# Optimization experiments

Hardware: AMD Instinct MI355X
Metric: run time of the kernel (lower is better)

Reference implementation:

```python
import jax, jax.numpy as jnp
import numpy as np

BSZ, H, P, L = 8, 512, 128, 8192
DT_MIN, DT_MAX = 1e-3, 1e-1


def setup_inputs() -> dict:
    key = jax.random.key(0)
    ks = jax.random.split(key, 6)
    inp = {}
    inp["input_sequence"] = jax.random.normal(ks[0], (BSZ, 1, H, 1, L), jnp.float32)
    # HiPPO-like init: negative real parts, pi*k imaginary parts
    inp["Lambda_re"] = -jax.random.uniform(ks[1], (P,), jnp.float32, 0.1, 1.0)
    inp["Lambda_im"] = jnp.pi * jnp.arange(P, dtype=jnp.float32)
    # lecun_normal-ish: fan_in = H for B, fan_in = P for C (real+imag parts)
    inp["B"] = jax.random.normal(ks[2], (P, H, 2), jnp.float32) / np.float32(np.sqrt(2 * H))
    inp["C"] = jax.random.normal(ks[3], (H, P, 2), jnp.float32) / np.float32(np.sqrt(2 * P))
    inp["D"] = jax.random.normal(ks[4], (H,), jnp.float32)
    u01 = jax.random.uniform(ks[5], (P, 1), jnp.float32)
    inp["log_step"] = u01 * np.float32(np.log(DT_MAX) - np.log(DT_MIN)) + np.float32(np.log(DT_MIN))
    return inp


def _binary_operator(q_i, q_j):
    A_i, b_i = q_i
    A_j, b_j = q_j
    return (A_j * A_i, A_j * b_i + b_j)


def reference(input_sequence, Lambda_re, Lambda_im, B, C, D, log_step):
    # (bsz, 1, H, 1, L) -> (bsz, L, H)
    u = input_sequence[:, 0, :, 0].transpose(0, 2, 1)

    Lambda = Lambda_re + 1j * Lambda_im                      # (P,)
    B_tilde = B[..., 0] + 1j * B[..., 1]                     # (P, H)
    C_tilde = C[..., 0] + 1j * C[..., 1]                     # (H, P)
    step = jnp.exp(log_step[:, 0])                           # (P,)

    # zero-order hold discretization
    Lambda_bar = jnp.exp(Lambda * step)                      # (P,)
    B_bar = ((Lambda_bar - 1.0) / Lambda)[:, None] * B_tilde # (P, H)

    Bu = jnp.einsum('blh,ph->blp', u, B_bar)                 # (bsz, L, P) complex
    Lambda_elems = jnp.broadcast_to(Lambda_bar, Bu.shape)
    _, xs = jax.lax.associative_scan(_binary_operator, (Lambda_elems, Bu), axis=1)

    # conj_sym=True -> factor of 2 on the real part of emissions
    ys = 2.0 * jnp.einsum('blp,hp->blh', xs, C_tilde).real + D * u
    ys = jax.nn.gelu(ys, approximate=False)

    # back to (bsz, 1, H, 1, L)
    return ys.transpose(0, 2, 1)[:, None, :, None, :]
```

## Files before the change

### kernel.cpp

```cpp
#include <hip/hip_runtime.h>
#include <hip/hip_bf16.h>
#include <cmath>

namespace {
constexpr int Pn = 128;
constexpr int Hn = 512;
constexpr int Ln = 8192;
constexpr int BS = 8;
constexpr size_t OFF_BMAT = 2048;
constexpr size_t OFF_CMAT = 264192;
constexpr size_t OFF_END  = 526336;
constexpr size_t OFF_CAR  = 2623488;
constexpr size_t HEADB    = 4720640;
constexpr size_t SZ_BU = (size_t)256 * Ln * 4;
}

typedef __attribute__((ext_vector_type(4))) float f32x4;
typedef __attribute__((ext_vector_type(8))) short bf16x8;
typedef __attribute__((ext_vector_type(4))) short bf16x4;

static __device__ inline short f2bf(float x) {
  __hip_bfloat16 h = __float2bfloat16(x);
  return *(short*)&h;
}

static __device__ inline void async_copy16(const void* g, void* l) {
  __builtin_amdgcn_global_load_lds(
      (const __attribute__((address_space(1))) unsigned int*)g,
      (__attribute__((address_space(3))) unsigned int*)l, 16, 0, 0);
}

__global__ void precompute_kernel(const float* __restrict__ Lre,
                                  const float* __restrict__ Lim,
                                  const float* __restrict__ Bin,
                                  const float* __restrict__ Cin,
                                  const float* __restrict__ lstep,
                                  float* __restrict__ Lam,
                                  __hip_bfloat16* __restrict__ Bmat,
                                  __hip_bfloat16* __restrict__ Cmat) {
  int tid = blockIdx.x * blockDim.x + threadIdx.x;
  if (tid < 2 * Pn * Hn) {
    int r = tid >> 9;
    int h = tid & (Hn - 1);
    int p = r & (Pn - 1);
    float st = expf(lstep[p]);
    float lr = Lre[p], li = Lim[p];
    float er = expf(lr * st);
    float cr = er * cosf(li * st);
    float ci = er * sinf(li * st);
    float nr = cr - 1.0f, ni = ci;
    float inv = 1.0f / (lr * lr + li * li);
    float wr = (nr * lr + ni * li) * inv;
    float wi = (ni * lr - nr * li) * inv;
    float btr = Bin[(p * Hn + h) * 2 + 0];
    float bti = Bin[(p * Hn + h) * 2 + 1];
    float val = (r < Pn) ? (wr * btr - wi * bti) : (wr * bti + wi * btr);
    Bmat[tid] = __float2bfloat16(val);
  } else if (tid < 4 * Pn * Hn) {
    int j = tid - 2 * Pn * Hn;
    int h = j >> 8;
    int c = j & 255;
    int p = c & (Pn - 1);
    float v = (c < Pn) ? 2.0f * Cin[(h * Pn + p) * 2 + 0]
                       : -2.0f * Cin[(h * Pn + p) * 2 + 1];
    Cmat[j] = __float2bfloat16(v);
  } else if (tid < 4 * Pn * Hn + 512) {
    int j = tid - 4 * Pn * Hn;
    int p = j & 127;
    int sel = j >> 7;
    float st = expf(lstep[p]);
    float lr = Lre[p], li = Lim[p];
    float sc = (sel < 2) ? st : 32.0f * st;
    float er = expf(lr * sc);
    Lam[(sel >> 1) * 256 + (sel & 1) * 128 + p] =
        (sel & 1) ? er * sinf(li * sc) : er * cosf(li * sc);
  }
}

__global__ __launch_bounds__(256) void gemm1_kernel(
    const __hip_bfloat16* __restrict__ Amat,
    const float* __restrict__ U,
    float* __restrict__ Bu,
    int b0) {
  __shared__ __align__(16) short As[256 * 32];
  __shared__ __align__(16) short Bs[64 * 40];
  const int t = threadIdx.x;
  const int lane = t & 63, w = t >> 6;
  const int n0 = blockIdx.x * 64;
  const int bz = blockIdx.z;
  const float* Ub = U + (size_t)(b0 + bz) * Hn * Ln;

  const int srow = lane >> 2, scol = (lane & 3) * 16;
  const int bn = t & 63, bkg = t >> 6;

  f32x4 acc[4][4] = {};
  for (int k0 = 0; k0 < Hn; k0 += 32) {
#pragma unroll
    for (int I2 = 0; I2 < 4; I2++) {
      int I = 4 * w + I2;
      async_copy16((const char*)(Amat + (size_t)(16 * I + srow) * Hn + k0) + scol,
                   (char*)As + I * 1024);
    }
    {
      float v[8];
#pragma unroll
      for (int j = 0; j < 8; j++)
        v[j] = Ub[(size_t)(k0 + bkg * 8 + j) * Ln + n0 + bn];
      bf16x8 pk;
#pragma unroll
      for (int j = 0; j < 8; j++) pk[j] = f2bf(v[j]);
      *(bf16x8*)&Bs[bn * 40 + bkg * 8] = pk;
    }
    __syncthreads();
    bf16x8 af[4], bfr[4];
#pragma unroll
    for (int mt = 0; mt < 4; mt++)
      af[mt] = *(const bf16x8*)&As[(64 * w + 16 * mt + (lane & 15)) * 32 + (lane >> 4) * 8];
#pragma unroll
    for (int nt = 0; nt < 4; nt++)
      bfr[nt] = *(const bf16x8*)&Bs[(16 * nt + (lane & 15)) * 40 + (lane >> 4) * 8];
#pragma unroll
    for (int mt = 0; mt < 4; mt++)
#pragma unroll
      for (int nt = 0; nt < 4; nt++)
        acc[mt][nt] = __builtin_amdgcn_mfma_f32_16x16x32_bf16(
            af[mt], bfr[nt], acc[mt][nt], 0, 0, 0);
    __syncthreads();
  }
  const int row4 = (lane >> 4) * 4, col = lane & 15;
  float* Bub = Bu + (size_t)bz * Ln * 256;
#pragma unroll
  for (int mt = 0; mt < 4; mt++)
#pragma unroll
    for (int nt = 0; nt < 4; nt++) {
      int n = n0 + 16 * nt + col;
      int m = 64 * w + 16 * mt + row4;
      *(f32x4*)&Bub[(size_t)n * 256 + m] = acc[mt][nt];
    }
}

__global__ __launch_bounds__(256) void scan_ends_kernel(const float* __restrict__ Bu,
                                                        const float* __restrict__ Lam,
                                                        float* __restrict__ End) {
  const int bz = blockIdx.y;
  const int t = threadIdx.x;
  const int c = blockIdx.x * 2 + (t >> 7);
  const int p = t & 127;
  const float Ar = Lam[p], Ai = Lam[128 + p];
  const float* base = Bu + ((size_t)bz * Ln + (size_t)c * 32) * 256;
  float br[32], bi[32];
#pragma unroll
  for (int i = 0; i < 32; i++) br[i] = base[(size_t)i * 256 + p];
#pragma unroll
  for (int i = 0; i < 32; i++) bi[i] = base[(size_t)i * 256 + 128 + p];
  float xr = 0.f, xi = 0.f;
#pragma unroll
  for (int i = 0; i < 32; i++) {
    float nr = fmaf(Ar, xr, fmaf(-Ai, xi, br[i]));
    float ni = fmaf(Ar, xi, fmaf(Ai, xr, bi[i]));
    xr = nr; xi = ni;
  }
  float* E = End + ((size_t)bz * 256 + c) * 256;
  E[p] = xr;
  E[128 + p] = xi;
}

__global__ __launch_bounds__(128) void carry_kernel(const float* __restrict__ End,
                                                    float* __restrict__ Carry,
                                                    const float* __restrict__ Lam) {
  const int bz = blockIdx.x;
  const int p = threadIdx.x;
  const float a32r = Lam[256 + p], a32i = Lam[384 + p];
  const float* E = End + (size_t)bz * 256 * 256;
  float* C = Carry + (size_t)bz * 256 * 256;
  float xr = 0.f, xi = 0.f;
  float er0[4], ei0[4], er1[4], ei1[4];
#pragma unroll
  for (int q = 0; q < 4; q++) {
    er0[q] = E[(size_t)q * 256 + p];
    ei0[q] = E[(size_t)q * 256 + 128 + p];
  }
  for (int c0 = 0; c0 < 256; c0 += 8) {
#pragma unroll
    for (int q = 0; q < 4; q++) {
      er1[q] = E[(size_t)(c0 + 4 + q) * 256 + p];
      ei1[q] = E[(size_t)(c0 + 4 + q) * 256 + 128 + p];
    }
#pragma unroll
    for (int q = 0; q < 4; q++) {
      C[(size_t)(c0 + q) * 256 + p] = xr;
      C[(size_t)(c0 + q) * 256 + 128 + p] = xi;
      float nr = fmaf(a32r, xr, fmaf(-a32i, xi, er0[q]));
      float ni = fmaf(a32r, xi, fmaf(a32i, xr, ei0[q]));
      xr = nr; xi = ni;
    }
#pragma unroll
    for (int q = 0; q < 4; q++) {
      int cn = c0 + 8 + q;
      if (cn < 256) {
        er0[q] = E[(size_t)cn * 256 + p];
        ei0[q] = E[(size_t)cn * 256 + 128 + p];
      }
    }
#pragma unroll
    for (int q = 0; q < 4; q++) {
      C[(size_t)(c0 + 4 + q) * 256 + p] = xr;
      C[(size_t)(c0 + 4 + q) * 256 + 128 + p] = xi;
      float nr = fmaf(a32r, xr, fmaf(-a32i, xi, er1[q]));
      float ni = fmaf(a32r, xi, fmaf(a32i, xr, ei1[q]));
      xr = nr; xi = ni;
    }
  }
}

__global__ __launch_bounds__(256) void scan_apply_kernel(float* __restrict__ Bu,
                                                         const float* __restrict__ Lam,
                                                         const float* __restrict__ Carry) {
  const int bz = blockIdx.y;
  const int t = threadIdx.x;
  const int c = blockIdx.x * 2 + (t >> 7);
  const int p = t & 127;
  const float Ar = Lam[p], Ai = Lam[128 + p];
  float* base = Bu + ((size_t)bz * Ln + (size_t)c * 32) * 256;
  const float* Cg = Carry + ((size_t)bz * 256 + c) * 256;
  float br[32], bi[32];
#pragma unroll
  for (int i = 0; i < 32; i++) br[i] = base[(size_t)i * 256 + p];
#pragma unroll
  for (int i = 0; i < 32; i++) bi[i] = base[(size_t)i * 256 + 128 + p];
  float xr = Cg[p], xi = Cg[128 + p];
#pragma unroll
  for (int i = 0; i < 32; i++) {
    float nr = fmaf(Ar, xr, fmaf(-Ai, xi, br[i]));
    float ni = fmaf(Ar, xi, fmaf(Ai, xr, bi[i]));
    xr = nr; xi = ni;
    base[(size_t)i * 256 + p] = nr;
    base[(size_t)i * 256 + 128 + p] = ni;
  }
}

__global__ __launch_bounds__(256) void gemm2_kernel(
    const __hip_bfloat16* __restrict__ Cmat,
    const float* __restrict__ Xs,
    const float* __restrict__ U,
    const float* __restrict__ Dv,
    float* __restrict__ Out, int b0) {
  __shared__ __align__(16) short As[128 * 32];
  __shared__ __align__(16) short Bs[128 * 40];
  const int t = threadIdx.x;
  const int lane = t & 63, w = t >> 6;
  const int wm = w >> 1, wn = w & 1;
  const int n0 = blockIdx.x * 128;
  const int m0 = blockIdx.y * 128;
  const int bz = blockIdx.z;
  const int b = b0 + bz;

  const int srow = lane >> 2, scol = (lane & 3) * 16;
  const int krow = t >> 2;
  const int kq = t & 3;
  const float* Xbase = Xs + ((size_t)bz * Ln + n0) * 256;

  f32x4 acc[4][4] = {};
  for (int k0 = 0; k0 < 256; k0 += 32) {
#pragma unroll
    for (int I2 = 0; I2 < 2; I2++) {
      int I = 2 * w + I2;
      async_copy16((const char*)(Cmat + (size_t)(m0 + 16 * I + srow) * 256 + k0) + scol,
                   (char*)As + I * 1024);
    }
#pragma unroll
    for (int ro = 0; ro < 2; ro++) {
      int row = ro * 64 + krow;
      const float* src = Xbase + (size_t)row * 256 + k0 + kq * 4;
      f32x4 x0 = *(const f32x4*)src;
      f32x4 x1 = *(const f32x4*)(src + 16);
      bf16x4 a, c;
#pragma unroll
      for (int q = 0; q < 4; q++) { a[q] = f2bf(x0[q]); c[q] = f2bf(x1[q]); }
      *(bf16x4*)&Bs[row * 40 + kq * 4] = a;
      *(bf16x4*)&Bs[row * 40 + 16 + kq * 4] = c;
    }
    __syncthreads();
    bf16x8 af[4], bfr[4];
#pragma unroll
    for (int mt = 0; mt < 4; mt++)
      af[mt] = *(const bf16x8*)&As[(64 * wm + 16 * mt + (lane & 15)) * 32 + (lane >> 4) * 8];
#pragma unroll
    for (int nt = 0; nt < 4; nt++)
      bfr[nt] = *(const bf16x8*)&Bs[(64 * wn + 16 * nt + (lane & 15)) * 40 + (lane >> 4) * 8];
#pragma unroll
    for (int mt = 0; mt < 4; mt++)
#pragma unroll
      for (int nt = 0; nt < 4; nt++)
        acc[mt][nt] = __builtin_amdgcn_mfma_f32_16x16x32_bf16(
            af[mt], bfr[nt], acc[mt][nt], 0, 0, 0);
    __syncthreads();
  }
  const int row4 = (lane >> 4) * 4, col = lane & 15;
#pragma unroll
  for (int mt = 0; mt < 4; mt++) {
#pragma unroll
    for (int r = 0; r < 4; r++) {
      int h = m0 + 64 * wm + 16 * mt + row4 + r;
      float dh = Dv[h];
      const float* Urow = U + ((size_t)b * Hn + h) * Ln;
      float* Orow = Out + ((size_t)b * Hn + h) * Ln;
#pragma unroll
      for (int nt = 0; nt < 4; nt++) {
        int n = n0 + 64 * wn + 16 * nt + col;
        float y = acc[mt][nt][r] + dh * Urow[n];
        float u2 = y * (0.7978845608f + 0.0356774081f * y * y);
        Orow[n] = y / (1.0f + __expf(-2.0f * u2));
      }
    }
  }
}

extern "C" void kernel_launch(void* const* d_in, const int* in_sizes, int n_in,
                              void* d_out, int out_size, void* d_ws, size_t ws_size,
                              hipStream_t stream) {
  const float* U   = (const float*)d_in[0];
  const float* Lre = (const float*)d_in[1];
  const float* Lim = (const float*)d_in[2];
  const float* Bin = (const float*)d_in[3];
  const float* Cin = (const float*)d_in[4];
  const float* Dv  = (const float*)d_in[5];
  const float* ls  = (const float*)d_in[6];
  float* out = (float*)d_out;

  char* wsb = (char*)d_ws;
  float* Lam = (float*)wsb;
  __hip_bfloat16* Bmat = (__hip_bfloat16*)(wsb + OFF_BMAT);
  __hip_bfloat16* Cmat = (__hip_bfloat16*)(wsb + OFF_CMAT);
  float* End = (float*)(wsb + OFF_END);
  float* Cy  = (float*)(wsb + OFF_CAR);
  float* Bu  = (float*)(wsb + HEADB);

  int NB = 8;
  while (NB > 1 && ws_size < HEADB + (size_t)NB * SZ_BU)
    NB >>= 1;

  precompute_kernel<<<(4 * Pn * Hn + 512 + 255) / 256, 256, 0, stream>>>(
      Lre, Lim, Bin, Cin, ls, Lam, Bmat, Cmat);

  for (int b0 = 0; b0 < BS; b0 += NB) {
    gemm1_kernel<<<dim3(Ln / 64, 1, NB), 256, 0, stream>>>(Bmat, U, Bu, b0);
    scan_ends_kernel<<<dim3(128, NB), 256, 0, stream>>>(Bu, Lam, End);
    carry_kernel<<<dim3(NB), 128, 0, stream>>>(End, Cy, Lam);
    scan_apply_kernel<<<dim3(128, NB), 256, 0, stream>>>(Bu, Lam, Cy);
    gemm2_kernel<<<dim3(Ln / 128, Hn / 128, NB), 256, 0, stream>>>(
        Cmat, Bu, U, Dv, out, b0);
  }
}
```

Before: 373.2 us.

## Emit bf16 scan output, load GEMM operands from global, double-buffer gemm1

scan_apply now writes the scanned states as bf16 in place (rows with a 512-short stride), and gemm2 reads those bf16 fragments and the C matrix straight from global memory, with no LDS staging or barriers. This halves the write and read traffic of the state tensor and drops the convert step in gemm2. gemm1 loads A fragments directly from global and double-buffers the converted U tile in LDS, so the next tile's loads overlap the MFMAs. Direct global fragment loads depend on cache hits, and the in-place bf16 write needs a block barrier so one thread's writes do not clobber rows another thread has not yet read.

New measurement: 430.4 us. 15.3% more time.

```diff
diff --git a/kernel.cpp b/kernel.cpp
--- a/kernel.cpp
+++ b/kernel.cpp
@@ -17,17 +17,10 @@
 
 typedef __attribute__((ext_vector_type(4))) float f32x4;
 typedef __attribute__((ext_vector_type(8))) short bf16x8;
-typedef __attribute__((ext_vector_type(4))) short bf16x4;
 
 static __device__ inline short f2bf(float x) {
   __hip_bfloat16 h = __float2bfloat16(x);
   return *(short*)&h;
-}
-
-static __device__ inline void async_copy16(const void* g, void* l) {
-  __builtin_amdgcn_global_load_lds(
-      (const __attribute__((address_space(1))) unsigned int*)g,
-      (__attribute__((address_space(3))) unsigned int*)l, 16, 0, 0);
 }
 
 __global__ void precompute_kernel(const float* __restrict__ Lre,
@@ -82,50 +75,59 @@
     const float* __restrict__ U,
     float* __restrict__ Bu,
     int b0) {
-  __shared__ __align__(16) short As[256 * 32];
-  __shared__ __align__(16) short Bs[64 * 40];
+  __shared__ __align__(16) short Bs[2][64 * 40];
   const int t = threadIdx.x;
   const int lane = t & 63, w = t >> 6;
   const int n0 = blockIdx.x * 64;
   const int bz = blockIdx.z;
   const float* Ub = U + (size_t)(b0 + bz) * Hn * Ln;
-
-  const int srow = lane >> 2, scol = (lane & 3) * 16;
+  const short* Ap = (const short*)Amat;
+  const int lr = lane & 15, lk = (lane >> 4) * 8;
   const int bn = t & 63, bkg = t >> 6;
 
+  {
+    float v[8];
+#pragma unroll
+    for (int j = 0; j < 8; j++)
+      v[j] = Ub[(size_t)(bkg * 8 + j) * Ln + n0 + bn];
+    bf16x8 pk;
+#pragma unroll
+    for (int j = 0; j < 8; j++) pk[j] = f2bf(v[j]);
+    *(bf16x8*)&Bs[0][bn * 40 + bkg * 8] = pk;
+  }
+  __syncthreads();
+
   f32x4 acc[4][4] = {};
-  for (int k0 = 0; k0 < Hn; k0 += 32) {
-#pragma unroll
-    for (int I2 = 0; I2 < 4; I2++) {
-      int I = 4 * w + I2;
-      async_copy16((const char*)(Amat + (size_t)(16 * I + srow) * Hn + k0) + scol,
-                   (char*)As + I * 1024);
-    }
-    {
-      float v[8];
+  int cur = 0;
+  for (int ks = 0; ks < 16; ks++) {
+    const int k0 = ks * 32;
+    float v[8];
+    if (ks < 15) {
 #pragma unroll
       for (int j = 0; j < 8; j++)
-        v[j] = Ub[(size_t)(k0 + bkg * 8 + j) * Ln + n0 + bn];
-      bf16x8 pk;
-#pragma unroll
-      for (int j = 0; j < 8; j++) pk[j] = f2bf(v[j]);
-      *(bf16x8*)&Bs[bn * 40 + bkg * 8] = pk;
-    }
-    __syncthreads();
+        v[j] = Ub[(size_t)(k0 + 32 + bkg * 8 + j) * Ln + n0 + bn];
+    }
     bf16x8 af[4], bfr[4];
 #pragma unroll
     for (int mt = 0; mt < 4; mt++)
-      af[mt] = *(const bf16x8*)&As[(64 * w + 16 * mt + (lane & 15)) * 32 + (lane >> 4) * 8];
+      af[mt] = *(const bf16x8*)&Ap[(size_t)(64 * w + 16 * mt + lr) * Hn + k0 + lk];
 #pragma unroll
     for (int nt = 0; nt < 4; nt++)
-      bfr[nt] = *(const bf16x8*)&Bs[(16 * nt + (lane & 15)) * 40 + (lane >> 4) * 8];
+      bfr[nt] = *(const bf16x8*)&Bs[cur][(16 * nt + lr) * 40 + lk];
 #pragma unroll
     for (int mt = 0; mt < 4; mt++)
 #pragma unroll
       for (int nt = 0; nt < 4; nt++)
         acc[mt][nt] = __builtin_amdgcn_mfma_f32_16x16x32_bf16(
             af[mt], bfr[nt], acc[mt][nt], 0, 0, 0);
+    if (ks < 15) {
+      bf16x8 pk;
+#pragma unroll
+      for (int j = 0; j < 8; j++) pk[j] = f2bf(v[j]);
+      *(bf16x8*)&Bs[cur ^ 1][bn * 40 + bkg * 8] = pk;
+    }
     __syncthreads();
+    cur ^= 1;
   }
   const int row4 = (lane >> 4) * 4, col = lane & 15;
   float* Bub = Bu + (size_t)bz * Ln * 256;
@@ -222,6 +224,7 @@
   const int p = t & 127;
   const float Ar = Lam[p], Ai = Lam[128 + p];
   float* base = Bu + ((size_t)bz * Ln + (size_t)c * 32) * 256;
+  short* outb = (short*)base;
   const float* Cg = Carry + ((size_t)bz * 256 + c) * 256;
   float br[32], bi[32];
 #pragma unroll
@@ -229,24 +232,23 @@
 #pragma unroll
   for (int i = 0; i < 32; i++) bi[i] = base[(size_t)i * 256 + 128 + p];
   float xr = Cg[p], xi = Cg[128 + p];
+  __syncthreads();
 #pragma unroll
   for (int i = 0; i < 32; i++) {
     float nr = fmaf(Ar, xr, fmaf(-Ai, xi, br[i]));
     float ni = fmaf(Ar, xi, fmaf(Ai, xr, bi[i]));
     xr = nr; xi = ni;
-    base[(size_t)i * 256 + p] = nr;
-    base[(size_t)i * 256 + 128 + p] = ni;
+    outb[(size_t)i * 512 + p] = f2bf(nr);
+    outb[(size_t)i * 512 + 128 + p] = f2bf(ni);
   }
 }
 
 __global__ __launch_bounds__(256) void gemm2_kernel(
     const __hip_bfloat16* __restrict__ Cmat,
-    const float* __restrict__ Xs,
+    const short* __restrict__ Xs,
     const float* __restrict__ U,
     const float* __restrict__ Dv,
     float* __restrict__ Out, int b0) {
-  __shared__ __align__(16) short As[128 * 32];
-  __shared__ __align__(16) short Bs[128 * 40];
   const int t = threadIdx.x;
   const int lane = t & 63, w = t >> 6;
   const int wm = w >> 1, wn = w & 1;
@@ -254,47 +256,27 @@
   const int m0 = blockIdx.y * 128;
   const int bz = blockIdx.z;
   const int b = b0 + bz;
-
-  const int srow = lane >> 2, scol = (lane & 3) * 16;
-  const int krow = t >> 2;
-  const int kq = t & 3;
-  const float* Xbase = Xs + ((size_t)bz * Ln + n0) * 256;
+  const int lr = lane & 15, lk = (lane >> 4) * 8;
+  const short* Ap = (const short*)Cmat;
+  const short* Bp = Xs + (size_t)bz * Ln * 512;
 
   f32x4 acc[4][4] = {};
-  for (int k0 = 0; k0 < 256; k0 += 32) {
-#pragma unroll
-    for (int I2 = 0; I2 < 2; I2++) {
-      int I = 2 * w + I2;
-      async_copy16((const char*)(Cmat + (size_t)(m0 + 16 * I + srow) * 256 + k0) + scol,
-                   (char*)As + I * 1024);
-    }
-#pragma unroll
-    for (int ro = 0; ro < 2; ro++) {
-      int row = ro * 64 + krow;
-      const float* src = Xbase + (size_t)row * 256 + k0 + kq * 4;
-      f32x4 x0 = *(const f32x4*)src;
-      f32x4 x1 = *(const f32x4*)(src + 16);
-      bf16x4 a, c;
-#pragma unroll
-      for (int q = 0; q < 4; q++) { a[q] = f2bf(x0[q]); c[q] = f2bf(x1[q]); }
-      *(bf16x4*)&Bs[row * 40 + kq * 4] = a;
-      *(bf16x4*)&Bs[row * 40 + 16 + kq * 4] = c;
-    }
-    __syncthreads();
+#pragma unroll
+  for (int ks = 0; ks < 8; ks++) {
+    const int k0 = ks * 32;
     bf16x8 af[4], bfr[4];
 #pragma unroll
     for (int mt = 0; mt < 4; mt++)
-      af[mt] = *(const bf16x8*)&As[(64 * wm + 16 * mt + (lane & 15)) * 32 + (lane >> 4) * 8];
+      af[mt] = *(const bf16x8*)&Ap[(size_t)(m0 + 64 * wm + 16 * mt + lr) * 256 + k0 + lk];
 #pragma unroll
     for (int nt = 0; nt < 4; nt++)
-      bfr[nt] = *(const bf16x8*)&Bs[(64 * wn + 16 * nt + (lane & 15)) * 40 + (lane >> 4) * 8];
+      bfr[nt] = *(const bf16x8*)&Bp[(size_t)(n0 + 64 * wn + 16 * nt + lr) * 512 + k0 + lk];
 #pragma unroll
     for (int mt = 0; mt < 4; mt++)
 #pragma unroll
       for (int nt = 0; nt < 4; nt++)
         acc[mt][nt] = __builtin_amdgcn_mfma_f32_16x16x32_bf16(
             af[mt], bfr[nt], acc[mt][nt], 0, 0, 0);
-    __syncthreads();
   }
   const int row4 = (lane >> 4) * 4, col = lane & 15;
 #pragma unroll
@@ -349,6 +331,6 @@
     carry_kernel<<<dim3(NB), 128, 0, stream>>>(End, Cy, Lam);
     scan_apply_kernel<<<dim3(128, NB), 256, 0, stream>>>(Bu, Lam, Cy);
     gemm2_kernel<<<dim3(Ln / 128, Hn / 128, NB), 256, 0, stream>>>(
-        Cmat, Bu, U, Dv, out, b0);
-  }
-}
+        Cmat, (const short*)Bu, U, Dv, out, b0);
+  }
+}
```

## Fuse local chunk scan into gemm1 and carry correction into gemm2

Applied to the files above, without the earlier changes.

Gemm1 now runs the per-chunk (64-step) linear recurrence in shared memory right after its MFMA accumulation, writing locally scanned states and chunk end values. This removes both the separate scan_ends and scan_apply passes over the large Bu buffer. Gemm2 applies the inter-chunk carry on the fly using precomputed powers of Lambda_bar (Ppow) before converting to bf16, and stages the whole K=256 tile in LDS once. The costs are a serial 32-step scan done by half the threads inside gemm1, a larger LDS footprint in both kernels, and gemm2 reading A fragments directly from global memory.

New measurement: 432.4 us. +15.9%, slower.

```diff
diff --git a/kernel.cpp b/kernel.cpp
--- a/kernel.cpp
+++ b/kernel.cpp
@@ -9,9 +9,10 @@
 constexpr int BS = 8;
 constexpr size_t OFF_BMAT = 2048;
 constexpr size_t OFF_CMAT = 264192;
-constexpr size_t OFF_END  = 526336;
-constexpr size_t OFF_CAR  = 2623488;
-constexpr size_t HEADB    = 4720640;
+constexpr size_t OFF_PPOW = 526336;
+constexpr size_t OFF_END  = 591872;
+constexpr size_t OFF_CAR  = 1640448;
+constexpr size_t HEADB    = 2689024;
 constexpr size_t SZ_BU = (size_t)256 * Ln * 4;
 }
 
@@ -37,7 +38,8 @@
                                   const float* __restrict__ lstep,
                                   float* __restrict__ Lam,
                                   __hip_bfloat16* __restrict__ Bmat,
-                                  __hip_bfloat16* __restrict__ Cmat) {
+                                  __hip_bfloat16* __restrict__ Cmat,
+                                  float* __restrict__ Ppow) {
   int tid = blockIdx.x * blockDim.x + threadIdx.x;
   if (tid < 2 * Pn * Hn) {
     int r = tid >> 9;
@@ -70,10 +72,20 @@
     int sel = j >> 7;
     float st = expf(lstep[p]);
     float lr = Lre[p], li = Lim[p];
-    float sc = (sel < 2) ? st : 32.0f * st;
+    float sc = (sel < 2) ? st : 64.0f * st;
     float er = expf(lr * sc);
     Lam[(sel >> 1) * 256 + (sel & 1) * 128 + p] =
         (sel & 1) ? er * sinf(li * sc) : er * cosf(li * sc);
+  } else if (tid < 4 * Pn * Hn + 512 + 64 * 256) {
+    int j = tid - 4 * Pn * Hn - 512;
+    int jr = j >> 8;
+    int k = j & 255;
+    int p = k & 127;
+    float st = expf(lstep[p]);
+    float lr = Lre[p], li = Lim[p];
+    float tt = st * (float)(jr + 1);
+    float er = expf(lr * tt);
+    Ppow[j] = (k < 128) ? er * cosf(li * tt) : er * sinf(li * tt);
   }
 }
 
@@ -81,9 +93,13 @@
     const __hip_bfloat16* __restrict__ Amat,
     const float* __restrict__ U,
     float* __restrict__ Bu,
+    float* __restrict__ End,
+    const float* __restrict__ Lam,
     int b0) {
-  __shared__ __align__(16) short As[256 * 32];
-  __shared__ __align__(16) short Bs[64 * 40];
+  __shared__ __align__(16) char shm[33280];
+  short* As = (short*)shm;
+  short* Bsb = (short*)(shm + 16384);
+  float (*Sl)[260] = (float(*)[260])shm;
   const int t = threadIdx.x;
   const int lane = t & 63, w = t >> 6;
   const int n0 = blockIdx.x * 64;
@@ -92,6 +108,7 @@
 
   const int srow = lane >> 2, scol = (lane & 3) * 16;
   const int bn = t & 63, bkg = t >> 6;
+  const int lr = lane & 15, lk = (lane >> 4) * 8;
 
   f32x4 acc[4][4] = {};
   for (int k0 = 0; k0 < Hn; k0 += 32) {
@@ -109,16 +126,16 @@
       bf16x8 pk;
 #pragma unroll
       for (int j = 0; j < 8; j++) pk[j] = f2bf(v[j]);
-      *(bf16x8*)&Bs[bn * 40 + bkg * 8] = pk;
+      *(bf16x8*)&Bsb[bn * 40 + bkg * 8] = pk;
     }
     __syncthreads();
     bf16x8 af[4], bfr[4];
 #pragma unroll
     for (int mt = 0; mt < 4; mt++)
-      af[mt] = *(const bf16x8*)&As[(64 * w + 16 * mt + (lane & 15)) * 32 + (lane >> 4) * 8];
+      af[mt] = *(const bf16x8*)&As[(64 * w + 16 * mt + lr) * 32 + lk];
 #pragma unroll
     for (int nt = 0; nt < 4; nt++)
-      bfr[nt] = *(const bf16x8*)&Bs[(16 * nt + (lane & 15)) * 40 + (lane >> 4) * 8];
+      bfr[nt] = *(const bf16x8*)&Bsb[(16 * nt + lr) * 40 + lk];
 #pragma unroll
     for (int mt = 0; mt < 4; mt++)
 #pragma unroll
@@ -127,42 +144,48 @@
             af[mt], bfr[nt], acc[mt][nt], 0, 0, 0);
     __syncthreads();
   }
+
   const int row4 = (lane >> 4) * 4, col = lane & 15;
   float* Bub = Bu + (size_t)bz * Ln * 256;
-#pragma unroll
-  for (int mt = 0; mt < 4; mt++)
-#pragma unroll
-    for (int nt = 0; nt < 4; nt++) {
-      int n = n0 + 16 * nt + col;
-      int m = 64 * w + 16 * mt + row4;
-      *(f32x4*)&Bub[(size_t)n * 256 + m] = acc[mt][nt];
-    }
-}
-
-__global__ __launch_bounds__(256) void scan_ends_kernel(const float* __restrict__ Bu,
-                                                        const float* __restrict__ Lam,
-                                                        float* __restrict__ End) {
-  const int bz = blockIdx.y;
-  const int t = threadIdx.x;
-  const int c = blockIdx.x * 2 + (t >> 7);
-  const int p = t & 127;
-  const float Ar = Lam[p], Ai = Lam[128 + p];
-  const float* base = Bu + ((size_t)bz * Ln + (size_t)c * 32) * 256;
-  float br[32], bi[32];
-#pragma unroll
-  for (int i = 0; i < 32; i++) br[i] = base[(size_t)i * 256 + p];
-#pragma unroll
-  for (int i = 0; i < 32; i++) bi[i] = base[(size_t)i * 256 + 128 + p];
-  float xr = 0.f, xi = 0.f;
-#pragma unroll
-  for (int i = 0; i < 32; i++) {
-    float nr = fmaf(Ar, xr, fmaf(-Ai, xi, br[i]));
-    float ni = fmaf(Ar, xi, fmaf(Ai, xr, bi[i]));
-    xr = nr; xi = ni;
-  }
-  float* E = End + ((size_t)bz * 256 + c) * 256;
-  E[p] = xr;
-  E[128 + p] = xi;
+  float scr = 0.f, sci = 0.f;
+  const float Ar = Lam[t & 127], Ai = Lam[128 + (t & 127)];
+#pragma unroll
+  for (int pass = 0; pass < 2; pass++) {
+    __syncthreads();
+#pragma unroll
+    for (int mt = 0; mt < 4; mt++)
+#pragma unroll
+      for (int ntl = 0; ntl < 2; ntl++) {
+        int nt = 2 * pass + ntl;
+        *(f32x4*)&Sl[16 * ntl + col][64 * w + 16 * mt + row4] = acc[mt][nt];
+      }
+    __syncthreads();
+    if (t < 128) {
+      const int p = t;
+#pragma unroll
+      for (int j = 0; j < 32; j++) {
+        float br = Sl[j][p], bi = Sl[j][128 + p];
+        float nr = fmaf(Ar, scr, fmaf(-Ai, sci, br));
+        float ni = fmaf(Ar, sci, fmaf(Ai, scr, bi));
+        scr = nr; sci = ni;
+        Sl[j][p] = nr; Sl[j][128 + p] = ni;
+      }
+    }
+    __syncthreads();
+    {
+      const int row = t >> 3, seg = t & 7;
+      float* dst = Bub + (size_t)(n0 + 32 * pass + row) * 256 + seg * 32;
+      const float* src = &Sl[row][seg * 32];
+#pragma unroll
+      for (int q = 0; q < 8; q++)
+        *(f32x4*)&dst[4 * q] = *(const f32x4*)&src[4 * q];
+    }
+  }
+  if (t < 128) {
+    float* E = End + ((size_t)bz * 128 + blockIdx.x) * 256;
+    E[t] = scr;
+    E[128 + t] = sci;
+  }
 }
 
 __global__ __launch_bounds__(128) void carry_kernel(const float* __restrict__ End,
@@ -170,9 +193,9 @@
                                                     const float* __restrict__ Lam) {
   const int bz = blockIdx.x;
   const int p = threadIdx.x;
-  const float a32r = Lam[256 + p], a32i = Lam[384 + p];
-  const float* E = End + (size_t)bz * 256 * 256;
-  float* C = Carry + (size_t)bz * 256 * 256;
+  const float a64r = Lam[256 + p], a64i = Lam[384 + p];
+  const float* E = End + (size_t)bz * 128 * 256;
+  float* C = Carry + (size_t)bz * 128 * 256;
   float xr = 0.f, xi = 0.f;
   float er0[4], ei0[4], er1[4], ei1[4];
 #pragma unroll
@@ -180,7 +203,7 @@
     er0[q] = E[(size_t)q * 256 + p];
     ei0[q] = E[(size_t)q * 256 + 128 + p];
   }
-  for (int c0 = 0; c0 < 256; c0 += 8) {
+  for (int c0 = 0; c0 < 128; c0 += 8) {
 #pragma unroll
     for (int q = 0; q < 4; q++) {
       er1[q] = E[(size_t)(c0 + 4 + q) * 256 + p];
@@ -190,14 +213,14 @@
     for (int q = 0; q < 4; q++) {
       C[(size_t)(c0 + q) * 256 + p] = xr;
       C[(size_t)(c0 + q) * 256 + 128 + p] = xi;
-      float nr = fmaf(a32r, xr, fmaf(-a32i, xi, er0[q]));
-      float ni = fmaf(a32r, xi, fmaf(a32i, xr, ei0[q]));
+      float nr = fmaf(a64r, xr, fmaf(-a64i, xi, er0[q]));
+      float ni = fmaf(a64r, xi, fmaf(a64i, xr, ei0[q]));
       xr = nr; xi = ni;
     }
 #pragma unroll
     for (int q = 0; q < 4; q++) {
       int cn = c0 + 8 + q;
-      if (cn < 256) {
+      if (cn < 128) {
         er0[q] = E[(size_t)cn * 256 + p];
         ei0[q] = E[(size_t)cn * 256 + 128 + p];
       }
@@ -206,47 +229,22 @@
     for (int q = 0; q < 4; q++) {
       C[(size_t)(c0 + 4 + q) * 256 + p] = xr;
       C[(size_t)(c0 + 4 + q) * 256 + 128 + p] = xi;
-      float nr = fmaf(a32r, xr, fmaf(-a32i, xi, er1[q]));
-      float ni = fmaf(a32r, xi, fmaf(a32i, xr, ei1[q]));
+      float nr = fmaf(a64r, xr, fmaf(-a64i, xi, er1[q]));
+      float ni = fmaf(a64r, xi, fmaf(a64i, xr, ei1[q]));
       xr = nr; xi = ni;
     }
-  }
-}
-
-__global__ __launch_bounds__(256) void scan_apply_kernel(float* __restrict__ Bu,
-                                                         const float* __restrict__ Lam,
-                                                         const float* __restrict__ Carry) {
-  const int bz = blockIdx.y;
-  const int t = threadIdx.x;
-  const int c = blockIdx.x * 2 + (t >> 7);
-  const int p = t & 127;
-  const float Ar = Lam[p], Ai = Lam[128 + p];
-  float* base = Bu + ((size_t)bz * Ln + (size_t)c * 32) * 256;
-  const float* Cg = Carry + ((size_t)bz * 256 + c) * 256;
-  float br[32], bi[32];
-#pragma unroll
-  for (int i = 0; i < 32; i++) br[i] = base[(size_t)i * 256 + p];
-#pragma unroll
-  for (int i = 0; i < 32; i++) bi[i] = base[(size_t)i * 256 + 128 + p];
-  float xr = Cg[p], xi = Cg[128 + p];
-#pragma unroll
-  for (int i = 0; i < 32; i++) {
-    float nr = fmaf(Ar, xr, fmaf(-Ai, xi, br[i]));
-    float ni = fmaf(Ar, xi, fmaf(Ai, xr, bi[i]));
-    xr = nr; xi = ni;
-    base[(size_t)i * 256 + p] = nr;
-    base[(size_t)i * 256 + 128 + p] = ni;
   }
 }
 
 __global__ __launch_bounds__(256) void gemm2_kernel(
     const __hip_bfloat16* __restrict__ Cmat,
     const float* __restrict__ Xs,
+    const float* __restrict__ Ppow,
+    const float* __restrict__ Cy,
     const float* __restrict__ U,
     const float* __restrict__ Dv,
     float* __restrict__ Out, int b0) {
-  __shared__ __align__(16) short As[128 * 32];
-  __shared__ __align__(16) short Bs[128 * 40];
+  __shared__ __align__(16) short BsF[128 * 264];
   const int t = threadIdx.x;
   const int lane = t & 63, w = t >> 6;
   const int wm = w >> 1, wn = w & 1;
@@ -254,48 +252,66 @@
   const int m0 = blockIdx.y * 128;
   const int bz = blockIdx.z;
   const int b = b0 + bz;
-
-  const int srow = lane >> 2, scol = (lane & 3) * 16;
-  const int krow = t >> 2;
-  const int kq = t & 3;
-  const float* Xbase = Xs + ((size_t)bz * Ln + n0) * 256;
-
+  const short* Ap = (const short*)Cmat;
+  const float* Xb = Xs + ((size_t)bz * Ln + n0) * 256;
+
+  {
+    const int kc = (t & 63) * 4;
+    const int rb = t >> 6;
+    const bool isRe = kc < 128;
+    const int p0 = kc & 127;
+    const float sgn = isRe ? -1.f : 1.f;
+    const float* Cyb = Cy + ((size_t)bz * 128 + 2 * blockIdx.x) * 256;
+    f32x4 ca[2], cb[2];
+#pragma unroll
+    for (int ch = 0; ch < 2; ch++) {
+      f32x4 cre = *(const f32x4*)&Cyb[ch * 256 + p0];
+      f32x4 cim = *(const f32x4*)&Cyb[ch * 256 + 128 + p0];
+      ca[ch] = isRe ? cre : cim;
+      f32x4 cbv = isRe ? cim : cre;
+      cb[ch] = cbv * sgn;
+    }
+#pragma unroll
+    for (int h = 0; h < 2; h++) {
+#pragma unroll
+      for (int i2 = 0; i2 < 16; i2++) {
+        int r = 64 * h + rb + 4 * i2;
+        int j = rb + 4 * i2;
+        f32x4 v = *(const f32x4*)&Xb[(size_t)r * 256 + kc];
+        f32x4 Pre = *(const f32x4*)&Ppow[j * 256 + p0];
+        f32x4 Pim = *(const f32x4*)&Ppow[j * 256 + 128 + p0];
+#pragma unroll
+        for (int q = 0; q < 4; q++)
+          v[q] = fmaf(Pre[q], ca[h][q], fmaf(Pim[q], cb[h][q], v[q]));
+        bf16x4 pk;
+#pragma unroll
+        for (int q = 0; q < 4; q++) pk[q] = f2bf(v[q]);
+        *(bf16x4*)&BsF[r * 264 + kc] = pk;
+      }
+    }
+  }
+  __syncthreads();
+
+  const int lr = lane & 15, lk = (lane >> 4) * 8;
   f32x4 acc[4][4] = {};
-  for (int k0 = 0; k0 < 256; k0 += 32) {
-#pragma unroll
-    for (int I2 = 0; I2 < 2; I2++) {
-      int I = 2 * w + I2;
-      async_copy16((const char*)(Cmat + (size_t)(m0 + 16 * I + srow) * 256 + k0) + scol,
-                   (char*)As + I * 1024);
-    }
-#pragma unroll
-    for (int ro = 0; ro < 2; ro++) {
-      int row = ro * 64 + krow;
-      const float* src = Xbase + (size_t)row * 256 + k0 + kq * 4;
-      f32x4 x0 = *(const f32x4*)src;
-      f32x4 x1 = *(const f32x4*)(src + 16);
-      bf16x4 a, c;
-#pragma unroll
-      for (int q = 0; q < 4; q++) { a[q] = f2bf(x0[q]); c[q] = f2bf(x1[q]); }
-      *(bf16x4*)&Bs[row * 40 + kq * 4] = a;
-      *(bf16x4*)&Bs[row * 40 + 16 + kq * 4] = c;
-    }
-    __syncthreads();
+#pragma unroll
+  for (int ks = 0; ks < 8; ks++) {
+    const int k0 = ks * 32;
     bf16x8 af[4], bfr[4];
 #pragma unroll
     for (int mt = 0; mt < 4; mt++)
-      af[mt] = *(const bf16x8*)&As[(64 * wm + 16 * mt + (lane & 15)) * 32 + (lane >> 4) * 8];
+      af[mt] = *(const bf16x8*)&Ap[(size_t)(m0 + 64 * wm + 16 * mt + lr) * 256 + k0 + lk];
 #pragma unroll
     for (int nt = 0; nt < 4; nt++)
-      bfr[nt] = *(const bf16x8*)&Bs[(64 * wn + 16 * nt + (lane & 15)) * 40 + (lane >> 4) * 8];
+      bfr[nt] = *(const bf16x8*)&BsF[(64 * wn + 16 * nt + lr) * 264 + k0 + lk];
 #pragma unroll
     for (int mt = 0; mt < 4; mt++)
 #pragma unroll
       for (int nt = 0; nt < 4; nt++)
         acc[mt][nt] = __builtin_amdgcn_mfma_f32_16x16x32_bf16(
             af[mt], bfr[nt], acc[mt][nt], 0, 0, 0);
-    __syncthreads();
-  }
+  }
+
   const int row4 = (lane >> 4) * 4, col = lane & 15;
 #pragma unroll
   for (int mt = 0; mt < 4; mt++) {
@@ -332,6 +348,7 @@
   float* Lam = (float*)wsb;
   __hip_bfloat16* Bmat = (__hip_bfloat16*)(wsb + OFF_BMAT);
   __hip_bfloat16* Cmat = (__hip_bfloat16*)(wsb + OFF_CMAT);
+  float* Ppow = (float*)(wsb + OFF_PPOW);
   float* End = (float*)(wsb + OFF_END);
   float* Cy  = (float*)(wsb + OFF_CAR);
   float* Bu  = (float*)(wsb + HEADB);
@@ -340,15 +357,13 @@
   while (NB > 1 && ws_size < HEADB + (size_t)NB * SZ_BU)
     NB >>= 1;
 
-  precompute_kernel<<<(4 * Pn * Hn + 512 + 255) / 256, 256, 0, stream>>>(
-      Lre, Lim, Bin, Cin, ls, Lam, Bmat, Cmat);
+  precompute_kernel<<<(4 * Pn * Hn + 512 + 64 * 256 + 255) / 256, 256, 0, stream>>>(
+      Lre, Lim, Bin, Cin, ls, Lam, Bmat, Cmat, Ppow);
 
   for (int b0 = 0; b0 < BS; b0 += NB) {
-    gemm1_kernel<<<dim3(Ln / 64, 1, NB), 256, 0, stream>>>(Bmat, U, Bu, b0);
-    scan_ends_kernel<<<dim3(128, NB), 256, 0, stream>>>(Bu, Lam, End);
+    gemm1_kernel<<<dim3(Ln / 64, 1, NB), 256, 0, stream>>>(Bmat, U, Bu, End, Lam, b0);
     carry_kernel<<<dim3(NB), 128, 0, stream>>>(End, Cy, Lam);
-    scan_apply_kernel<<<dim3(128, NB), 256, 0, stream>>>(Bu, Lam, Cy);
     gemm2_kernel<<<dim3(Ln / 128, Hn / 128, NB), 256, 0, stream>>>(
-        Cmat, Bu, U, Dv, out, b0);
-  }
-}
+        Cmat, Bu, Ppow, Cy, U, Dv, out, b0);
+  }
+}
```
